# Kernel optimization log

Hardware: AMD Instinct MI355X
Metric: run time of the kernel (lower is better)

Reference implementation:

```python
import jax, jax.numpy as jnp
import numpy as np

BN_EPS = 1e-5

def setup_inputs() -> dict:
    key = jax.random.key(0)
    ks = jax.random.split(key, 8)
    N, E, D = 50000, 800000, 128
    x = jax.random.normal(ks[0], (N, D), dtype=jnp.float32)
    edge_index = jax.random.randint(ks[1], (2, E), 0, N, dtype=jnp.int64)
    s = 1.0 / np.sqrt(D)
    W1 = jax.random.uniform(ks[2], (D, D), jnp.float32, -s, s)
    b1 = jax.random.uniform(ks[3], (D,), jnp.float32, -s, s)
    W2 = jax.random.uniform(ks[4], (D, D), jnp.float32, -s, s)
    b2 = jax.random.uniform(ks[5], (D,), jnp.float32, -s, s)
    g1 = jnp.ones((D,), jnp.float32); be1 = jnp.zeros((D,), jnp.float32)
    g2 = jnp.ones((D,), jnp.float32); be2 = jnp.zeros((D,), jnp.float32)
    eps = jnp.zeros((), jnp.float32)  # learnable GIN epsilon (train_eps=True)
    return {"x": x, "edge_index": edge_index, "eps": eps,
            "W1": W1, "b1": b1, "g1": g1, "be1": be1,
            "W2": W2, "b2": b2, "g2": g2, "be2": be2}

def _batchnorm(h, gamma, beta):
    # training-mode BatchNorm1d over node axis (biased variance)
    mu = jnp.mean(h, axis=0)
    var = jnp.mean(jnp.square(h - mu), axis=0)
    return (h - mu) * jax.lax.rsqrt(var + BN_EPS) * gamma + beta

def reference(x, edge_index, eps, W1, b1, g1, be1, W2, b2, g2, be2):
    N = x.shape[0]
    src, dst = edge_index[0], edge_index[1]
    # GIN aggregation: sum of neighbor features (scatter-add to target nodes)
    agg = jax.ops.segment_sum(x[src], dst, num_segments=N)  # [N, D]
    h = (1.0 + eps) * x + agg
    # MLP: Linear -> BN -> ReLU -> Linear
    h = h @ W1.T + b1
    h = jax.nn.relu(_batchnorm(h, g1, be1))
    h = h @ W2.T + b2
    # outer BatchNorm + ReLU
    return jax.nn.relu(_batchnorm(h, g2, be2))
```

## Files before the change

### kernel.cpp

```cpp
#include <hip/hip_runtime.h>
#include <hip/hip_bf16.h>


#define DIM 128
#define SUB 2
#define CAP 32
#define KMAX 64

typedef unsigned short u16;
typedef __attribute__((ext_vector_type(8))) short short8;
typedef __attribute__((ext_vector_type(4))) float f32x4;

__device__ inline u16 f2b(float f) {
  unsigned int u = __builtin_bit_cast(unsigned int, f);
  u += 0x7fffu + ((u >> 16) & 1u);
  return (u16)(u >> 16);
}
__device__ inline float b2f(u16 b) {
  unsigned int u = ((unsigned int)b) << 16;
  return __builtin_bit_cast(float, u);
}

__global__ __launch_bounds__(256) void prep_kernel(
    const float* __restrict__ W1, const float* __restrict__ W2,
    const float* __restrict__ x, int* __restrict__ cursor,
    u16* __restrict__ wb1, u16* __restrict__ wb2, u16* __restrict__ xb,
    int Z, int NX) {
  int i = blockIdx.x * blockDim.x + threadIdx.x;
  const int stride = gridDim.x * blockDim.x;
  const int e1 = Z + 4096, e2 = Z + 8192, e3 = Z + 8192 + NX;
  for (; i < e3; i += stride) {
    if (i < Z) {
      int4 z = {0, 0, 0, 0};
      reinterpret_cast<int4*>(cursor)[i] = z;
    } else if (i < e1) {
      const int j = i - Z;
      const float4 v = reinterpret_cast<const float4*>(W1)[j];
      ushort4 o = {f2b(v.x), f2b(v.y), f2b(v.z), f2b(v.w)};
      reinterpret_cast<ushort4*>(wb1)[j] = o;
    } else if (i < e2) {
      const int j = i - e1;
      const float4 v = reinterpret_cast<const float4*>(W2)[j];
      ushort4 o = {f2b(v.x), f2b(v.y), f2b(v.z), f2b(v.w)};
      reinterpret_cast<ushort4*>(wb2)[j] = o;
    } else {
      const int j = i - e2;
      const float4 v = reinterpret_cast<const float4*>(x)[j];
      ushort4 o = {f2b(v.x), f2b(v.y), f2b(v.z), f2b(v.w)};
      reinterpret_cast<ushort4*>(xb)[j] = o;
    }
  }
}

__global__ __launch_bounds__(256) void reorder_kernel(
    const int* __restrict__ ei, int* __restrict__ cursor,
    u16* __restrict__ buckets, int E) {
  const int t = blockIdx.x * blockDim.x + threadIdx.x;
  const int stride = gridDim.x * blockDim.x;
  const int way = t & 1;
  for (int e = t; e < E; e += 2 * stride) {
    const int e2 = e + stride;
    const int s1 = ei[e], d1 = ei[E + e];
    const bool v2 = e2 < E;
    int s2 = 0, d2 = 0;
    if (v2) { s2 = ei[e2]; d2 = ei[E + e2]; }
    const int p1 = atomicAdd(&cursor[d1 * SUB + way], 1);
    const int p2 = v2 ? atomicAdd(&cursor[d2 * SUB + way], 1) : 0;
    if (p1 < CAP) buckets[d1 * KMAX + way * CAP + p1] = (u16)s1;
    if (v2 && p2 < CAP) buckets[d2 * KMAX + way * CAP + p2] = (u16)s2;
  }
}

__global__ __launch_bounds__(256) void aggregate_kernel(
    const u16* __restrict__ xb, const int* __restrict__ cursor,
    const u16* __restrict__ buckets, const float* __restrict__ epsp,
    u16* __restrict__ hb, int N) {
  const int g = threadIdx.x >> 5;
  const int lane = threadIdx.x & 31;
  const int node = blockIdx.x * 8 + g;
  if (node >= N) return;
  const float k = 1.0f + epsp[0];
  int c0 = cursor[node * SUB + 0]; if (c0 > CAP) c0 = CAP;
  int c1 = cursor[node * SUB + 1]; if (c1 > CAP) c1 = CAP;
  const u16* bk = buckets + node * KMAX;

  const ushort4 xv = *reinterpret_cast<const ushort4*>(xb + (long long)node * DIM + lane * 4);
  float ax = k * b2f(xv.x), ay = k * b2f(xv.y), az = k * b2f(xv.z), aw = k * b2f(xv.w);

#pragma unroll
  for (int w = 0; w < SUB; ++w) {
    const int d = w ? c1 : c0;
    const u16* b = bk + w * CAP;
    int j = 0;
    for (; j + 4 <= d; j += 4) {
      const int s0 = b[j], s1 = b[j + 1], s2 = b[j + 2], s3 = b[j + 3];
      const ushort4 v0 = *reinterpret_cast<const ushort4*>(xb + (long long)s0 * DIM + lane * 4);
      const ushort4 v1 = *reinterpret_cast<const ushort4*>(xb + (long long)s1 * DIM + lane * 4);
      const ushort4 v2 = *reinterpret_cast<const ushort4*>(xb + (long long)s2 * DIM + lane * 4);
      const ushort4 v3 = *reinterpret_cast<const ushort4*>(xb + (long long)s3 * DIM + lane * 4);
      ax += b2f(v0.x) + b2f(v1.x) + b2f(v2.x) + b2f(v3.x);
      ay += b2f(v0.y) + b2f(v1.y) + b2f(v2.y) + b2f(v3.y);
      az += b2f(v0.z) + b2f(v1.z) + b2f(v2.z) + b2f(v3.z);
      aw += b2f(v0.w) + b2f(v1.w) + b2f(v2.w) + b2f(v3.w);
    }
    for (; j < d; ++j) {
      const int s = b[j];
      const ushort4 v = *reinterpret_cast<const ushort4*>(xb + (long long)s * DIM + lane * 4);
      ax += b2f(v.x); ay += b2f(v.y); az += b2f(v.z); aw += b2f(v.w);
    }
  }
  ushort4 o = {f2b(ax), f2b(ay), f2b(az), f2b(aw)};
  *reinterpret_cast<ushort4*>(hb + (long long)node * DIM + lane * 4) = o;
}

template <int FUSE>
__global__ __launch_bounds__(256) void gemm_mfma_kernel(
    const void* __restrict__ Av, const u16* __restrict__ Wb,
    const float* __restrict__ bias, const float* __restrict__ ss,
    float* __restrict__ C, float* __restrict__ stats, int N) {
  __shared__ float sred[4][DIM];
  __shared__ float qred[4][DIM];
  const int lane = threadIdx.x & 63;
  const int wid = threadIdx.x >> 6;
  const int l15 = lane & 15;
  const int lg = lane >> 4;
  const int wrow = blockIdx.x * 64 + wid * 16;

  f32x4 acc[8];
#pragma unroll
  for (int ni = 0; ni < 8; ++ni) acc[ni] = (f32x4){0.f, 0.f, 0.f, 0.f};

  int arow = wrow + l15;
  if (arow >= N) arow = N - 1;

#pragma unroll
  for (int kb = 0; kb < 4; ++kb) {
    const int k0 = kb * 32 + lg * 8;
    short8 a;
    if (FUSE) {
      const float* A = (const float*)Av + (long long)arow * DIM + k0;
      const float4 v0 = *reinterpret_cast<const float4*>(A);
      const float4 v1 = *reinterpret_cast<const float4*>(A + 4);
      const float4 sc0 = *reinterpret_cast<const float4*>(ss + k0);
      const float4 sc1 = *reinterpret_cast<const float4*>(ss + k0 + 4);
      const float4 sh0 = *reinterpret_cast<const float4*>(ss + DIM + k0);
      const float4 sh1 = *reinterpret_cast<const float4*>(ss + DIM + k0 + 4);
      a[0] = (short)f2b(fmaxf(fmaf(v0.x, sc0.x, sh0.x), 0.f));
      a[1] = (short)f2b(fmaxf(fmaf(v0.y, sc0.y, sh0.y), 0.f));
      a[2] = (short)f2b(fmaxf(fmaf(v0.z, sc0.z, sh0.z), 0.f));
      a[3] = (short)f2b(fmaxf(fmaf(v0.w, sc0.w, sh0.w), 0.f));
      a[4] = (short)f2b(fmaxf(fmaf(v1.x, sc1.x, sh1.x), 0.f));
      a[5] = (short)f2b(fmaxf(fmaf(v1.y, sc1.y, sh1.y), 0.f));
      a[6] = (short)f2b(fmaxf(fmaf(v1.z, sc1.z, sh1.z), 0.f));
      a[7] = (short)f2b(fmaxf(fmaf(v1.w, sc1.w, sh1.w), 0.f));
    } else {
      a = *reinterpret_cast<const short8*>((const u16*)Av + (long long)arow * DIM + k0);
    }
#pragma unroll
    for (int ni = 0; ni < 8; ++ni) {
      const short8 b = *reinterpret_cast<const short8*>(Wb + (ni * 16 + l15) * DIM + k0);
      acc[ni] = __builtin_amdgcn_mfma_f32_16x16x32_bf16(a, b, acc[ni], 0, 0, 0);
    }
  }

  const int rbase = wrow + lg * 4;
#pragma unroll
  for (int ni = 0; ni < 8; ++ni) {
    const int col = ni * 16 + l15;
    const float bv = bias[col];
    float s = 0.f, q = 0.f;
#pragma unroll
    for (int r = 0; r < 4; ++r) {
      const int row = rbase + r;
      if (row < N) {
        const float v = acc[ni][r] + bv;
        C[(long long)row * DIM + col] = v;
        s += v;
        q = fmaf(v, v, q);
      }
    }
    s += __shfl_xor(s, 16); s += __shfl_xor(s, 32);
    q += __shfl_xor(q, 16); q += __shfl_xor(q, 32);
    if (lg == 0) { sred[wid][col] = s; qred[wid][col] = q; }
  }
  __syncthreads();
  const int t = threadIdx.x;
  if (t < DIM) {
    unsafeAtomicAdd(&stats[t], sred[0][t] + sred[1][t] + sred[2][t] + sred[3][t]);
  } else {
    const int c = t - DIM;
    unsafeAtomicAdd(&stats[DIM + c], qred[0][c] + qred[1][c] + qred[2][c] + qred[3][c]);
  }
}

__global__ void finalize_kernel(const float* __restrict__ stats,
                                const float* __restrict__ gamma,
                                const float* __restrict__ beta,
                                float* __restrict__ ss, float Ninv) {
  const int j = threadIdx.x;
  const float mu = stats[j] * Ninv;
  const float var = stats[DIM + j] * Ninv - mu * mu;
  const float sc = gamma[j] * rsqrtf(var + 1e-5f);
  ss[j] = sc;
  ss[DIM + j] = beta[j] - mu * sc;
}

__global__ __launch_bounds__(256) void bnrelu_kernel(
    float* __restrict__ out, const float* __restrict__ ss, int total4) {
  float4* __restrict__ o4 = reinterpret_cast<float4*>(out);
  int i = blockIdx.x * blockDim.x + threadIdx.x;
  const int stride = gridDim.x * blockDim.x;
  for (; i < total4; i += stride) {
    const int c0 = (i * 4) & (DIM - 1);
    float4 v = o4[i];
    v.x = fmaxf(fmaf(v.x, ss[c0 + 0], ss[DIM + c0 + 0]), 0.f);
    v.y = fmaxf(fmaf(v.y, ss[c0 + 1], ss[DIM + c0 + 1]), 0.f);
    v.z = fmaxf(fmaf(v.z, ss[c0 + 2], ss[DIM + c0 + 2]), 0.f);
    v.w = fmaxf(fmaf(v.w, ss[c0 + 3], ss[DIM + c0 + 3]), 0.f);
    o4[i] = v;
  }
}

extern "C" void kernel_launch(void* const* d_in, const int* in_sizes, int n_in,
                              void* d_out, int out_size, void* d_ws, size_t ws_size,
                              hipStream_t stream) {
  const float* x   = (const float*)d_in[0];
  const int*   ei  = (const int*)d_in[1];
  const float* eps = (const float*)d_in[2];
  const float* W1  = (const float*)d_in[3];
  const float* b1  = (const float*)d_in[4];
  const float* g1  = (const float*)d_in[5];
  const float* be1 = (const float*)d_in[6];
  const float* W2  = (const float*)d_in[7];
  const float* b2  = (const float*)d_in[8];
  const float* g2  = (const float*)d_in[9];
  const float* be2 = (const float*)d_in[10];
  float* out = (float*)d_out;

  const int N = in_sizes[0] / DIM;
  const int E = in_sizes[1] / 2;

  u16* hb      = (u16*)d_ws;
  u16* wb1     = hb + (size_t)N * DIM;
  u16* wb2     = wb1 + DIM * DIM;
  u16* buckets = wb2 + DIM * DIM;
  int* cursor  = (int*)(buckets + (size_t)N * KMAX);
  float* stats1 = (float*)(cursor + SUB * N);
  float* ss1    = stats1 + 256;
  float* stats2 = ss1 + 256;
  float* ss2    = stats2 + 256;

  u16* xb = (u16*)d_out;

  const int Z  = (SUB * N + 1024 + 3) / 4;
  const int NX = N * DIM / 4;

  prep_kernel<<<2048, 256, 0, stream>>>(W1, W2, x, cursor, wb1, wb2, xb, Z, NX);
  reorder_kernel<<<2048, 256, 0, stream>>>(ei, cursor, buckets, E);
  aggregate_kernel<<<(N + 7) / 8, 256, 0, stream>>>(xb, cursor, buckets, eps, hb, N);

  const int gblocks = (N + 63) / 64;
  gemm_mfma_kernel<0><<<gblocks, 256, 0, stream>>>(hb, wb1, b1, nullptr, out, stats1, N);
  finalize_kernel<<<1, DIM, 0, stream>>>(stats1, g1, be1, ss1, 1.0f / N);
  gemm_mfma_kernel<1><<<gblocks, 256, 0, stream>>>(out, wb2, b2, ss1, out, stats2, N);
  finalize_kernel<<<1, DIM, 0, stream>>>(stats2, g2, be2, ss2, 1.0f / N);
  bnrelu_kernel<<<2048, 256, 0, stream>>>(out, ss2, N * (DIM / 4));
}
```

Before: 274.0 us.

## Fuse BN finalize into consumers, bf16 second GEMM output, restructure gather and reorder

Drops the two finalize kernels: the GEMM and bnrelu kernels now compute the BN scale and shift into shared memory themselves. The second GEMM writes bf16 into the hb workspace, and bnrelu expands it to fp32 output, which cuts intermediate traffic. Aggregation now uses one 64-lane wave per node, with lanes holding neighbor indices that are shuffled to 4 slots loading 16-byte chunks, and a cross-slot reduction at the end. The reorder kernel gives each thread 8 edges and issues all loads and atomics up front. Risks are the extra bf16 rounding of the pre-BN activations and fewer independent loads in flight per node during the gather.

New measurement: 260.4 us. 1.05x faster.

```diff
diff --git a/kernel.cpp b/kernel.cpp
--- a/kernel.cpp
+++ b/kernel.cpp
@@ -9,6 +9,7 @@
 
 typedef unsigned short u16;
 typedef __attribute__((ext_vector_type(8))) short short8;
+typedef __attribute__((ext_vector_type(8))) unsigned short ushort8;
 typedef __attribute__((ext_vector_type(4))) float f32x4;
 
 __device__ inline u16 f2b(float f) {
@@ -54,72 +55,95 @@
 
 __global__ __launch_bounds__(256) void reorder_kernel(
     const int* __restrict__ ei, int* __restrict__ cursor,
-    u16* __restrict__ buckets, int E) {
+    u16* __restrict__ buckets, int E, int T) {
   const int t = blockIdx.x * blockDim.x + threadIdx.x;
-  const int stride = gridDim.x * blockDim.x;
   const int way = t & 1;
-  for (int e = t; e < E; e += 2 * stride) {
-    const int e2 = e + stride;
-    const int s1 = ei[e], d1 = ei[E + e];
-    const bool v2 = e2 < E;
-    int s2 = 0, d2 = 0;
-    if (v2) { s2 = ei[e2]; d2 = ei[E + e2]; }
-    const int p1 = atomicAdd(&cursor[d1 * SUB + way], 1);
-    const int p2 = v2 ? atomicAdd(&cursor[d2 * SUB + way], 1) : 0;
-    if (p1 < CAP) buckets[d1 * KMAX + way * CAP + p1] = (u16)s1;
-    if (v2 && p2 < CAP) buckets[d2 * KMAX + way * CAP + p2] = (u16)s2;
-  }
+  int s[8], d[8], p[8];
+  bool valid[8];
+#pragma unroll
+  for (int i = 0; i < 8; ++i) {
+    const int e = t + i * T;
+    valid[i] = e < E;
+    const int ec = valid[i] ? e : 0;
+    s[i] = ei[ec];
+    d[i] = ei[E + ec];
+  }
+#pragma unroll
+  for (int i = 0; i < 8; ++i)
+    p[i] = valid[i] ? atomicAdd(&cursor[d[i] * SUB + way], 1) : CAP;
+#pragma unroll
+  for (int i = 0; i < 8; ++i)
+    if (p[i] < CAP) buckets[d[i] * KMAX + way * CAP + p[i]] = (u16)s[i];
 }
 
 __global__ __launch_bounds__(256) void aggregate_kernel(
     const u16* __restrict__ xb, const int* __restrict__ cursor,
     const u16* __restrict__ buckets, const float* __restrict__ epsp,
     u16* __restrict__ hb, int N) {
-  const int g = threadIdx.x >> 5;
-  const int lane = threadIdx.x & 31;
-  const int node = blockIdx.x * 8 + g;
+  const int wid = threadIdx.x >> 6;
+  const int lane = threadIdx.x & 63;
+  const int node = blockIdx.x * 4 + wid;
   if (node >= N) return;
-  const float k = 1.0f + epsp[0];
+  const int slot = lane >> 4;
+  const int chunk = lane & 15;
   int c0 = cursor[node * SUB + 0]; if (c0 > CAP) c0 = CAP;
   int c1 = cursor[node * SUB + 1]; if (c1 > CAP) c1 = CAP;
+  const int deg = c0 + c1;
   const u16* bk = buckets + node * KMAX;
 
-  const ushort4 xv = *reinterpret_cast<const ushort4*>(xb + (long long)node * DIM + lane * 4);
-  float ax = k * b2f(xv.x), ay = k * b2f(xv.y), az = k * b2f(xv.z), aw = k * b2f(xv.w);
-
-#pragma unroll
-  for (int w = 0; w < SUB; ++w) {
-    const int d = w ? c1 : c0;
-    const u16* b = bk + w * CAP;
-    int j = 0;
-    for (; j + 4 <= d; j += 4) {
-      const int s0 = b[j], s1 = b[j + 1], s2 = b[j + 2], s3 = b[j + 3];
-      const ushort4 v0 = *reinterpret_cast<const ushort4*>(xb + (long long)s0 * DIM + lane * 4);
-      const ushort4 v1 = *reinterpret_cast<const ushort4*>(xb + (long long)s1 * DIM + lane * 4);
-      const ushort4 v2 = *reinterpret_cast<const ushort4*>(xb + (long long)s2 * DIM + lane * 4);
-      const ushort4 v3 = *reinterpret_cast<const ushort4*>(xb + (long long)s3 * DIM + lane * 4);
-      ax += b2f(v0.x) + b2f(v1.x) + b2f(v2.x) + b2f(v3.x);
-      ay += b2f(v0.y) + b2f(v1.y) + b2f(v2.y) + b2f(v3.y);
-      az += b2f(v0.z) + b2f(v1.z) + b2f(v2.z) + b2f(v3.z);
-      aw += b2f(v0.w) + b2f(v1.w) + b2f(v2.w) + b2f(v3.w);
-    }
-    for (; j < d; ++j) {
-      const int s = b[j];
-      const ushort4 v = *reinterpret_cast<const ushort4*>(xb + (long long)s * DIM + lane * 4);
-      ax += b2f(v.x); ay += b2f(v.y); az += b2f(v.z); aw += b2f(v.w);
-    }
-  }
-  ushort4 o = {f2b(ax), f2b(ay), f2b(az), f2b(aw)};
-  *reinterpret_cast<ushort4*>(hb + (long long)node * DIM + lane * 4) = o;
+  int my = 0;
+  if (lane < c0) my = bk[lane];
+  else if (lane - c0 < c1) my = bk[CAP + lane - c0];
+
+  float acc[8];
+#pragma unroll
+  for (int f = 0; f < 8; ++f) acc[f] = 0.f;
+
+  for (int t0 = 0; t0 < deg; t0 += 4) {
+    const int idx = t0 + slot;
+    const int src = __shfl(my, idx);
+    const ushort8 v = *reinterpret_cast<const ushort8*>(xb + (size_t)src * DIM + chunk * 8);
+    if (idx < deg) {
+#pragma unroll
+      for (int f = 0; f < 8; ++f) acc[f] += b2f(v[f]);
+    }
+  }
+#pragma unroll
+  for (int f = 0; f < 8; ++f) {
+    acc[f] += __shfl_xor(acc[f], 16);
+    acc[f] += __shfl_xor(acc[f], 32);
+  }
+  if (slot == 0) {
+    const float k = 1.0f + epsp[0];
+    const ushort8 xv = *reinterpret_cast<const ushort8*>(xb + (size_t)node * DIM + chunk * 8);
+    ushort8 o;
+#pragma unroll
+    for (int f = 0; f < 8; ++f) o[f] = f2b(acc[f] + k * b2f(xv[f]));
+    *reinterpret_cast<ushort8*>(hb + (size_t)node * DIM + chunk * 8) = o;
+  }
 }
 
 template <int FUSE>
 __global__ __launch_bounds__(256) void gemm_mfma_kernel(
     const void* __restrict__ Av, const u16* __restrict__ Wb,
-    const float* __restrict__ bias, const float* __restrict__ ss,
-    float* __restrict__ C, float* __restrict__ stats, int N) {
+    const float* __restrict__ bias, const float* __restrict__ statsIn,
+    const float* __restrict__ gamma, const float* __restrict__ beta,
+    void* __restrict__ Cv, float* __restrict__ statsOut, int N, float Ninv) {
   __shared__ float sred[4][DIM];
   __shared__ float qred[4][DIM];
+  __shared__ float ssc[DIM];
+  __shared__ float ssh[DIM];
+  if (FUSE) {
+    const int t = threadIdx.x;
+    if (t < DIM) {
+      const float mu = statsIn[t] * Ninv;
+      const float var = statsIn[DIM + t] * Ninv - mu * mu;
+      const float sc = gamma[t] * rsqrtf(var + 1e-5f);
+      ssc[t] = sc;
+      ssh[t] = beta[t] - mu * sc;
+    }
+    __syncthreads();
+  }
   const int lane = threadIdx.x & 63;
   const int wid = threadIdx.x >> 6;
   const int l15 = lane & 15;
@@ -138,23 +162,19 @@
     const int k0 = kb * 32 + lg * 8;
     short8 a;
     if (FUSE) {
-      const float* A = (const float*)Av + (long long)arow * DIM + k0;
+      const float* A = (const float*)Av + (size_t)arow * DIM + k0;
       const float4 v0 = *reinterpret_cast<const float4*>(A);
       const float4 v1 = *reinterpret_cast<const float4*>(A + 4);
-      const float4 sc0 = *reinterpret_cast<const float4*>(ss + k0);
-      const float4 sc1 = *reinterpret_cast<const float4*>(ss + k0 + 4);
-      const float4 sh0 = *reinterpret_cast<const float4*>(ss + DIM + k0);
-      const float4 sh1 = *reinterpret_cast<const float4*>(ss + DIM + k0 + 4);
-      a[0] = (short)f2b(fmaxf(fmaf(v0.x, sc0.x, sh0.x), 0.f));
-      a[1] = (short)f2b(fmaxf(fmaf(v0.y, sc0.y, sh0.y), 0.f));
-      a[2] = (short)f2b(fmaxf(fmaf(v0.z, sc0.z, sh0.z), 0.f));
-      a[3] = (short)f2b(fmaxf(fmaf(v0.w, sc0.w, sh0.w), 0.f));
-      a[4] = (short)f2b(fmaxf(fmaf(v1.x, sc1.x, sh1.x), 0.f));
-      a[5] = (short)f2b(fmaxf(fmaf(v1.y, sc1.y, sh1.y), 0.f));
-      a[6] = (short)f2b(fmaxf(fmaf(v1.z, sc1.z, sh1.z), 0.f));
-      a[7] = (short)f2b(fmaxf(fmaf(v1.w, sc1.w, sh1.w), 0.f));
+      a[0] = (short)f2b(fmaxf(fmaf(v0.x, ssc[k0 + 0], ssh[k0 + 0]), 0.f));
+      a[1] = (short)f2b(fmaxf(fmaf(v0.y, ssc[k0 + 1], ssh[k0 + 1]), 0.f));
+      a[2] = (short)f2b(fmaxf(fmaf(v0.z, ssc[k0 + 2], ssh[k0 + 2]), 0.f));
+      a[3] = (short)f2b(fmaxf(fmaf(v0.w, ssc[k0 + 3], ssh[k0 + 3]), 0.f));
+      a[4] = (short)f2b(fmaxf(fmaf(v1.x, ssc[k0 + 4], ssh[k0 + 4]), 0.f));
+      a[5] = (short)f2b(fmaxf(fmaf(v1.y, ssc[k0 + 5], ssh[k0 + 5]), 0.f));
+      a[6] = (short)f2b(fmaxf(fmaf(v1.z, ssc[k0 + 6], ssh[k0 + 6]), 0.f));
+      a[7] = (short)f2b(fmaxf(fmaf(v1.w, ssc[k0 + 7], ssh[k0 + 7]), 0.f));
     } else {
-      a = *reinterpret_cast<const short8*>((const u16*)Av + (long long)arow * DIM + k0);
+      a = *reinterpret_cast<const short8*>((const u16*)Av + (size_t)arow * DIM + k0);
     }
 #pragma unroll
     for (int ni = 0; ni < 8; ++ni) {
@@ -174,9 +194,17 @@
       const int row = rbase + r;
       if (row < N) {
         const float v = acc[ni][r] + bv;
-        C[(long long)row * DIM + col] = v;
-        s += v;
-        q = fmaf(v, v, q);
+        if (FUSE) {
+          const u16 bb = f2b(v);
+          const float vr = b2f(bb);
+          ((u16*)Cv)[(size_t)row * DIM + col] = bb;
+          s += vr;
+          q = fmaf(vr, vr, q);
+        } else {
+          ((float*)Cv)[(size_t)row * DIM + col] = v;
+          s += v;
+          q = fmaf(v, v, q);
+        }
       }
     }
     s += __shfl_xor(s, 16); s += __shfl_xor(s, 32);
@@ -186,38 +214,46 @@
   __syncthreads();
   const int t = threadIdx.x;
   if (t < DIM) {
-    unsafeAtomicAdd(&stats[t], sred[0][t] + sred[1][t] + sred[2][t] + sred[3][t]);
+    unsafeAtomicAdd(&statsOut[t], sred[0][t] + sred[1][t] + sred[2][t] + sred[3][t]);
   } else {
     const int c = t - DIM;
-    unsafeAtomicAdd(&stats[DIM + c], qred[0][c] + qred[1][c] + qred[2][c] + qred[3][c]);
-  }
-}
-
-__global__ void finalize_kernel(const float* __restrict__ stats,
-                                const float* __restrict__ gamma,
-                                const float* __restrict__ beta,
-                                float* __restrict__ ss, float Ninv) {
-  const int j = threadIdx.x;
-  const float mu = stats[j] * Ninv;
-  const float var = stats[DIM + j] * Ninv - mu * mu;
-  const float sc = gamma[j] * rsqrtf(var + 1e-5f);
-  ss[j] = sc;
-  ss[DIM + j] = beta[j] - mu * sc;
+    unsafeAtomicAdd(&statsOut[DIM + c], qred[0][c] + qred[1][c] + qred[2][c] + qred[3][c]);
+  }
 }
 
 __global__ __launch_bounds__(256) void bnrelu_kernel(
-    float* __restrict__ out, const float* __restrict__ ss, int total4) {
-  float4* __restrict__ o4 = reinterpret_cast<float4*>(out);
+    const u16* __restrict__ hb, float* __restrict__ out,
+    const float* __restrict__ stats, const float* __restrict__ gamma,
+    const float* __restrict__ beta, float Ninv, int total8) {
+  __shared__ float ssc[DIM];
+  __shared__ float ssh[DIM];
+  {
+    const int t = threadIdx.x;
+    if (t < DIM) {
+      const float mu = stats[t] * Ninv;
+      const float var = stats[DIM + t] * Ninv - mu * mu;
+      const float sc = gamma[t] * rsqrtf(var + 1e-5f);
+      ssc[t] = sc;
+      ssh[t] = beta[t] - mu * sc;
+    }
+    __syncthreads();
+  }
   int i = blockIdx.x * blockDim.x + threadIdx.x;
   const int stride = gridDim.x * blockDim.x;
-  for (; i < total4; i += stride) {
-    const int c0 = (i * 4) & (DIM - 1);
-    float4 v = o4[i];
-    v.x = fmaxf(fmaf(v.x, ss[c0 + 0], ss[DIM + c0 + 0]), 0.f);
-    v.y = fmaxf(fmaf(v.y, ss[c0 + 1], ss[DIM + c0 + 1]), 0.f);
-    v.z = fmaxf(fmaf(v.z, ss[c0 + 2], ss[DIM + c0 + 2]), 0.f);
-    v.w = fmaxf(fmaf(v.w, ss[c0 + 3], ss[DIM + c0 + 3]), 0.f);
-    o4[i] = v;
+  for (; i < total8; i += stride) {
+    const int c0 = (i * 8) & (DIM - 1);
+    const ushort8 v = reinterpret_cast<const ushort8*>(hb)[i];
+    float4 o0, o1;
+    o0.x = fmaxf(fmaf(b2f(v[0]), ssc[c0 + 0], ssh[c0 + 0]), 0.f);
+    o0.y = fmaxf(fmaf(b2f(v[1]), ssc[c0 + 1], ssh[c0 + 1]), 0.f);
+    o0.z = fmaxf(fmaf(b2f(v[2]), ssc[c0 + 2], ssh[c0 + 2]), 0.f);
+    o0.w = fmaxf(fmaf(b2f(v[3]), ssc[c0 + 3], ssh[c0 + 3]), 0.f);
+    o1.x = fmaxf(fmaf(b2f(v[4]), ssc[c0 + 4], ssh[c0 + 4]), 0.f);
+    o1.y = fmaxf(fmaf(b2f(v[5]), ssc[c0 + 5], ssh[c0 + 5]), 0.f);
+    o1.z = fmaxf(fmaf(b2f(v[6]), ssc[c0 + 6], ssh[c0 + 6]), 0.f);
+    o1.w = fmaxf(fmaf(b2f(v[7]), ssc[c0 + 7], ssh[c0 + 7]), 0.f);
+    reinterpret_cast<float4*>(out)[i * 2] = o0;
+    reinterpret_cast<float4*>(out)[i * 2 + 1] = o1;
   }
 }
 
@@ -246,23 +282,26 @@
   u16* buckets = wb2 + DIM * DIM;
   int* cursor  = (int*)(buckets + (size_t)N * KMAX);
   float* stats1 = (float*)(cursor + SUB * N);
-  float* ss1    = stats1 + 256;
-  float* stats2 = ss1 + 256;
-  float* ss2    = stats2 + 256;
+  float* stats2 = stats1 + 256;
 
   u16* xb = (u16*)d_out;
 
-  const int Z  = (SUB * N + 1024 + 3) / 4;
+  const int Z  = (SUB * N + 512 + 3) / 4;
   const int NX = N * DIM / 4;
+  const float Ninv = 1.0f / N;
 
   prep_kernel<<<2048, 256, 0, stream>>>(W1, W2, x, cursor, wb1, wb2, xb, Z, NX);
-  reorder_kernel<<<2048, 256, 0, stream>>>(ei, cursor, buckets, E);
-  aggregate_kernel<<<(N + 7) / 8, 256, 0, stream>>>(xb, cursor, buckets, eps, hb, N);
+
+  const int nth = (E + 7) / 8;
+  const int rblocks = (nth + 255) / 256;
+  reorder_kernel<<<rblocks, 256, 0, stream>>>(ei, cursor, buckets, E, rblocks * 256);
+
+  aggregate_kernel<<<(N + 3) / 4, 256, 0, stream>>>(xb, cursor, buckets, eps, hb, N);
 
   const int gblocks = (N + 63) / 64;
-  gemm_mfma_kernel<0><<<gblocks, 256, 0, stream>>>(hb, wb1, b1, nullptr, out, stats1, N);
-  finalize_kernel<<<1, DIM, 0, stream>>>(stats1, g1, be1, ss1, 1.0f / N);
-  gemm_mfma_kernel<1><<<gblocks, 256, 0, stream>>>(out, wb2, b2, ss1, out, stats2, N);
-  finalize_kernel<<<1, DIM, 0, stream>>>(stats2, g2, be2, ss2, 1.0f / N);
-  bnrelu_kernel<<<2048, 256, 0, stream>>>(out, ss2, N * (DIM / 4));
-}
+  gemm_mfma_kernel<0><<<gblocks, 256, 0, stream>>>(
+      hb, wb1, b1, nullptr, nullptr, nullptr, (float*)d_out, stats1, N, Ninv);
+  gemm_mfma_kernel<1><<<gblocks, 256, 0, stream>>>(
+      (float*)d_out, wb2, b2, stats1, g1, be1, hb, stats2, N, Ninv);
+  bnrelu_kernel<<<2048, 256, 0, stream>>>(hb, out, stats2, g2, be2, Ninv, N * (DIM / 8));
+}
```
